# Kernel tuning notes

Hardware: AMD Instinct MI355X
Metric: run time of the kernel (lower is better)

## Reference

```python
import jax, jax.numpy as jnp
import numpy as np
from jax import lax

DIM = 96
HEADS = 3
EPS = 1e-12


def conv1x1(x, w):
    # x: [b,c,h,w], w: [o,c]
    return jnp.einsum('bchw,oc->bohw', x, w)


def dwconv3(x, w):
    # depthwise 3x3, SAME padding. w: [C,1,3,3]
    C = x.shape[1]
    return lax.conv_general_dilated(
        x, w, window_strides=(1, 1), padding='SAME',
        feature_group_count=C,
        dimension_numbers=('NCHW', 'OIHW', 'NCHW'))


def channel_attn(q, kv, temperature):
    # q: [b,C,h,w], kv: [b,2C,h,w], temperature: [heads,1,1]
    k, v = jnp.split(kv, 2, axis=1)
    b, C, h, w = q.shape
    c = C // HEADS
    r = lambda x: x.reshape(b, HEADS, c, h * w)
    q, k, v = r(q), r(k), r(v)
    # L2-normalize along the (h*w) axis (torch F.normalize semantics)
    qn = q / jnp.maximum(jnp.linalg.norm(q, axis=-1, keepdims=True), EPS)
    kn = k / jnp.maximum(jnp.linalg.norm(k, axis=-1, keepdims=True), EPS)
    attn = jnp.einsum('bhcn,bhdn->bhcd', qn, kn) * temperature  # [b,heads,c,c]
    attn = jax.nn.softmax(attn, axis=-1)
    out = jnp.einsum('bhcd,bhdn->bhcn', attn, v)
    return out.reshape(b, C, h, w)


def setup_inputs() -> dict:
    key = jax.random.key(0)
    ks = jax.random.split(key, 16)
    d = DIM
    s = lambda fan: 1.0 / np.sqrt(fan)
    inp = {
        'low': jax.random.normal(ks[0], (2, d, 256, 256), jnp.float32),
        'high': jax.random.normal(ks[1], (2, d, 256, 256), jnp.float32),
        'temperature': jnp.ones((HEADS, 1, 1), jnp.float32),
        'qc_w': jax.random.normal(ks[2], (d, d), jnp.float32) * s(d),
        'qdw_c_w': jax.random.normal(ks[3], (d, 1, 3, 3), jnp.float32) * s(9),
        'kvc_w': jax.random.normal(ks[4], (2 * d, d), jnp.float32) * s(d),
        'kvdw_c_w': jax.random.normal(ks[5], (2 * d, 1, 3, 3), jnp.float32) * s(9),
        'qt_w': jax.random.normal(ks[6], (d, d), jnp.float32) * s(d),
        'qdw_t_w': jax.random.normal(ks[7], (d, 1, 3, 3), jnp.float32) * s(9),
        'kvt_w': jax.random.normal(ks[8], (2 * d, d), jnp.float32) * s(d),
        'kvdw_t_w': jax.random.normal(ks[9], (2 * d, 1, 3, 3), jnp.float32) * s(9),
        'po_c_w': jax.random.normal(ks[10], (d, d), jnp.float32) * s(d),
        'po_t_w': jax.random.normal(ks[11], (d, d), jnp.float32) * s(d),
        'concat_w': jax.random.normal(ks[12], (d, 2 * d), jnp.float32) * s(2 * d),
        'concat_b': jax.random.normal(ks[13], (d,), jnp.float32) * s(2 * d),
    }
    return inp


def reference(low, high, temperature, qc_w, qdw_c_w, kvc_w, kvdw_c_w,
              qt_w, qdw_t_w, kvt_w, kvdw_t_w, po_c_w, po_t_w,
              concat_w, concat_b):
    q_c = dwconv3(conv1x1(high, qc_w), qdw_c_w)
    kv_c = dwconv3(conv1x1(high, kvc_w), kvdw_c_w)
    q_t = dwconv3(conv1x1(low, qt_w), qdw_t_w)
    kv_t = dwconv3(conv1x1(low, kvt_w), kvdw_t_w)
    out_c = conv1x1(channel_attn(q_c, kv_t, temperature), po_c_w)
    out_t = conv1x1(channel_attn(q_t, kv_c, temperature), po_t_w)
    out = jnp.concatenate([out_c, out_t], axis=1)
    out = conv1x1(out, concat_w) + concat_b[None, :, None, None]
    return out
```

## Files before the change

### kernel.cpp

```cpp
#include <hip/hip_runtime.h>
#include <hip/hip_bf16.h>

#define HW 65536
#define GNS 64

typedef __attribute__((ext_vector_type(8))) short short8;
typedef __attribute__((ext_vector_type(4))) float f32x4;
union U8 { short8 s; unsigned u[4]; ushort h[8]; };

static __device__ __forceinline__ ushort f2bf(float f) {
    union { float f; unsigned u; } v; v.f = f;
    unsigned u = v.u;
    unsigned r = (u + 0x7fffu + ((u >> 16) & 1u)) >> 16;
    return (ushort)r;
}
static __device__ __forceinline__ float bf2f(ushort u) {
    union { unsigned u; float f; } v; v.u = ((unsigned)u) << 16; return v.f;
}
static __device__ __forceinline__ unsigned pk2(float a, float b) {
    __hip_bfloat162 h = __float22bfloat162_rn(make_float2(a, b));
    union { __hip_bfloat162 h; unsigned u; } c; c.h = h; return c.u;
}
static __device__ __forceinline__ f32x4 mfma16(short8 a, short8 b, f32x4 c) {
    return __builtin_amdgcn_mfma_f32_16x16x32_bf16(a, b, c, 0, 0, 0);
}

__global__ __launch_bounds__(256) void prep_kernel(
        const float* __restrict__ qc, const float* __restrict__ kvc,
        const float* __restrict__ qt, const float* __restrict__ kvt,
        const float* __restrict__ cw, const float* __restrict__ poc, const float* __restrict__ pot,
        ushort* __restrict__ Wc, ushort* __restrict__ Wt,
        float* __restrict__ W1, float* __restrict__ W2, float* __restrict__ SSQ) {
    int bx = blockIdx.x, tid = threadIdx.x;
    if (bx < 9) {
        for (int idx = bx * 256 + tid; idx < 288 * 96; idx += 9 * 256) {
            Wc[idx] = f2bf(idx < 96 * 96 ? qc[idx] : kvc[idx - 96 * 96]);
            Wt[idx] = f2bf(idx < 96 * 96 ? qt[idx] : kvt[idx - 96 * 96]);
        }
        if (bx == 0)
            for (int idx = tid; idx < 8 * 96; idx += 256) SSQ[idx] = 0.f;
    } else {
        int idx = (bx - 9) * 256 + tid;
        int sel = idx < 9216 ? 0 : 1;
        int i = sel ? idx - 9216 : idx;
        int o = i / 96, m = i % 96;
        const float* po = sel ? pot : poc;
        float acc = 0.f;
        for (int p = 0; p < 96; ++p)
            acc += cw[o * 192 + sel * 96 + p] * po[p * 96 + m];
        (sel ? W2 : W1)[i] = acc;
    }
}

__global__ __launch_bounds__(256, 2) void conv_kernel(
        const float* __restrict__ Xc, const float* __restrict__ Xt,
        const ushort* __restrict__ Wcp, const ushort* __restrict__ Wtp,
        ushort* __restrict__ Yco, ushort* __restrict__ Yto) {
    __shared__ ushort xs[96][136];
    int strm = blockIdx.z;
    const float* X = strm ? Xt : Xc;
    const ushort* W = strm ? Wtp : Wcp;
    ushort* Y = strm ? Yto : Yco;
    int tid = threadIdx.x;
    int n0 = blockIdx.x * 128;
    int b = blockIdx.y;
    int wave = tid >> 6, lane = tid & 63, lr = lane & 15, lg = lane >> 4;
    const float* Xb = X + (size_t)b * 96 * HW + n0;
    #pragma unroll
    for (int i = 0; i < 12; ++i) {
        int idx = tid + i * 256;
        int ch = idx >> 5, g = idx & 31;
        float4 v = *(const float4*)(Xb + (size_t)ch * HW + 4 * g);
        unsigned* d = (unsigned*)&xs[ch][4 * g];
        d[0] = pk2(v.x, v.y);
        d[1] = pk2(v.z, v.w);
    }
    __syncthreads();
    short8 af[2][3];
    #pragma unroll
    for (int nt = 0; nt < 2; ++nt) {
        int n = wave * 32 + nt * 16 + lr;
        #pragma unroll
        for (int kk = 0; kk < 3; ++kk) {
            int kb = kk * 32 + lg * 8;
            U8 t;
            #pragma unroll
            for (int j = 0; j < 4; ++j) {
                unsigned e0 = xs[kb + 2 * j][n];
                unsigned e1 = xs[kb + 2 * j + 1][n];
                t.u[j] = e0 | (e1 << 16);
            }
            af[nt][kk] = t.s;
        }
    }
    __syncthreads();
    ushort* ys = &xs[0][0];
    int row0 = tid >> 4, g = tid & 15;
    for (int og = 0; og < 3; ++og) {
        const ushort* Wg = W + (size_t)og * 96 * 96 + (size_t)lr * 96 + lg * 8;
        #pragma unroll
        for (int mt = 0; mt < 6; ++mt) {
            f32x4 a0 = {0.f, 0.f, 0.f, 0.f}, a1 = {0.f, 0.f, 0.f, 0.f};
            #pragma unroll
            for (int kk = 0; kk < 3; ++kk) {
                short8 wf = *(const short8*)(Wg + (size_t)mt * 16 * 96 + kk * 32);
                a0 = mfma16(af[0][kk], wf, a0);
                a1 = mfma16(af[1][kk], wf, a1);
            }
            unsigned* d0 = (unsigned*)&ys[(mt * 16 + lr) * 136 + wave * 32 + lg * 4];
            d0[0] = pk2(a0[0], a0[1]);
            d0[1] = pk2(a0[2], a0[3]);
            unsigned* d1 = (unsigned*)&ys[(mt * 16 + lr) * 136 + wave * 32 + 16 + lg * 4];
            d1[0] = pk2(a1[0], a1[1]);
            d1[1] = pk2(a1[2], a1[3]);
        }
        __syncthreads();
        ushort* Yg = Y + (size_t)(b * 288 + og * 96) * HW + n0;
        #pragma unroll
        for (int p = 0; p < 6; ++p) {
            int row = p * 16 + row0;
            *(short8*)&Yg[(size_t)row * HW + 8 * g] = *(const short8*)&ys[row * 136 + 8 * g];
        }
        __syncthreads();
    }
}

__global__ __launch_bounds__(256, 8) void dw_kernel(
        const ushort* __restrict__ Yc, const ushort* __restrict__ Yt,
        const float* __restrict__ qdw_c, const float* __restrict__ kvdw_c,
        const float* __restrict__ qdw_t, const float* __restrict__ kvdw_t,
        ushort* __restrict__ QKVc, ushort* __restrict__ QKVt,
        float* __restrict__ SSQ, int base_strm) {
    int tid = threadIdx.x, wave = tid >> 6, lane = tid & 63;
    int strm = base_strm + blockIdx.z;
    int ch = blockIdx.y % 288, b = blockIdx.y / 288;
    int r0 = blockIdx.x * 32 + wave * 8;
    const ushort* Y = strm ? Yt : Yc;
    ushort* QKV = strm ? QKVt : QKVc;
    const float* qdw = strm ? qdw_t : qdw_c;
    const float* kvdw = strm ? kvdw_t : kvdw_c;
    const float* w = (ch < 96) ? (qdw + ch * 9) : (kvdw + (ch - 96) * 9);
    float w00 = w[0], w01 = w[1], w02 = w[2], w10 = w[3], w11 = w[4],
          w12 = w[5], w20 = w[6], w21 = w[7], w22 = w[8];
    const ushort* src = Y + (size_t)(b * 288 + ch) * HW;
    float rows[3][6];
    float ssq = 0.f;
    #define LOADROW(R, D)                                                    \
    {                                                                        \
        int r_ = (R);                                                        \
        if ((unsigned)r_ < 256u) {                                           \
            ushort4 t4 = *(const ushort4*)(src + r_ * 256 + 4 * lane);       \
            float c0 = bf2f(t4.x), c1 = bf2f(t4.y), c2 = bf2f(t4.z), c3 = bf2f(t4.w); \
            float lft = __shfl(c3, lane - 1);                                \
            float rgt = __shfl(c0, lane + 1);                                \
            if (lane == 0) lft = 0.f;                                        \
            if (lane == 63) rgt = 0.f;                                       \
            D[0] = lft; D[1] = c0; D[2] = c1; D[3] = c2; D[4] = c3; D[5] = rgt; \
        } else {                                                             \
            D[0] = 0.f; D[1] = 0.f; D[2] = 0.f; D[3] = 0.f; D[4] = 0.f; D[5] = 0.f; \
        }                                                                    \
    }
    LOADROW(r0 - 1, rows[0]);
    LOADROW(r0, rows[1]);
    ushort* dst = QKV + (size_t)(b * 288 + ch) * HW;
    #pragma unroll
    for (int orow = 0; orow < 8; ++orow) {
        LOADROW(r0 + orow + 1, rows[(orow + 2) % 3]);
        float* ra = rows[orow % 3];
        float* rb = rows[(orow + 1) % 3];
        float* rc = rows[(orow + 2) % 3];
        float acc[4];
        #pragma unroll
        for (int j = 0; j < 4; ++j) {
            acc[j] = w00 * ra[j] + w01 * ra[j + 1] + w02 * ra[j + 2]
                   + w10 * rb[j] + w11 * rb[j + 1] + w12 * rb[j + 2]
                   + w20 * rc[j] + w21 * rc[j + 1] + w22 * rc[j + 2];
            ssq += acc[j] * acc[j];
        }
        uint2 pv;
        pv.x = pk2(acc[0], acc[1]);
        pv.y = pk2(acc[2], acc[3]);
        *(uint2*)&dst[(r0 + orow) * 256 + 4 * lane] = pv;
    }
    #undef LOADROW
    if (ch < 192) {
        #pragma unroll
        for (int off = 1; off < 64; off <<= 1) ssq += __shfl_xor(ssq, off);
        if (lane == 0) {
            int t_ = ch >= 96;
            int chq = t_ ? ch - 96 : ch;
            int a_ = (strm == 0) ? t_ : (1 - t_);
            atomicAdd(&SSQ[((a_ * 2 + b) * 2 + t_) * 96 + chq], ssq);
        }
    }
}

__global__ __launch_bounds__(256) void gram_kernel(const ushort* __restrict__ QKVc,
                                                   const ushort* __restrict__ QKVt,
                                                   float* __restrict__ Gpart) {
    __shared__ ushort qs[32 * 256];
    __shared__ ushort ks2[32 * 256];
    __shared__ float Gp[4][32][32];
    int tid = threadIdx.x, wave = tid >> 6, lane = tid & 63;
    int lr = lane & 15, lg = lane >> 4;
    int code = blockIdx.y;
    int a = code / 6, b = (code % 6) / 3, h = code % 3;
    const ushort* qsrc = (a == 0) ? QKVc : QKVt;
    const ushort* ksrc = (a == 0) ? QKVt : QKVc;
    const ushort* qb = qsrc + (size_t)(b * 288 + 32 * h) * HW + blockIdx.x * 1024;
    const ushort* kb = ksrc + (size_t)(b * 288 + 96 + 32 * h) * HW + blockIdx.x * 1024;
    f32x4 acc[2][2];
    #pragma unroll
    for (int i = 0; i < 2; ++i)
        #pragma unroll
        for (int j = 0; j < 2; ++j) acc[i][j] = (f32x4){0.f, 0.f, 0.f, 0.f};
    for (int ph = 0; ph < 4; ++ph) {
        int noff = ph * 256;
        #pragma unroll
        for (int i = 0; i < 4; ++i) {
            int idx = tid + i * 256;
            int row = idx >> 5, g = idx & 31;
            int col = (g * 8) ^ ((row & 7) << 3);
            *(short8*)&qs[row * 256 + col] = *(const short8*)(qb + (size_t)row * HW + noff + 8 * g);
            *(short8*)&ks2[row * 256 + col] = *(const short8*)(kb + (size_t)row * HW + noff + 8 * g);
        }
        __syncthreads();
        #pragma unroll
        for (int j = 0; j < 2; ++j) {
            int ks_ = wave * 2 + j;
            int c0 = (ks_ * 32 + lg * 8) ^ ((lr & 7) << 3);
            short8 a0 = *(const short8*)&qs[lr * 256 + c0];
            short8 a1 = *(const short8*)&qs[(16 + lr) * 256 + c0];
            short8 b0 = *(const short8*)&ks2[lr * 256 + c0];
            short8 b1 = *(const short8*)&ks2[(16 + lr) * 256 + c0];
            acc[0][0] = mfma16(a0, b0, acc[0][0]);
            acc[0][1] = mfma16(a0, b1, acc[0][1]);
            acc[1][0] = mfma16(a1, b0, acc[1][0]);
            acc[1][1] = mfma16(a1, b1, acc[1][1]);
        }
        __syncthreads();
    }
    #pragma unroll
    for (int i = 0; i < 2; ++i)
        #pragma unroll
        for (int j = 0; j < 2; ++j)
            #pragma unroll
            for (int r = 0; r < 4; ++r)
                Gp[wave][i * 16 + lg * 4 + r][j * 16 + lr] = acc[i][j][r];
    __syncthreads();
    float* Gout = Gpart + ((size_t)code * GNS + blockIdx.x) * 1024;
    for (int idx = tid; idx < 1024; idx += 256) {
        float ssum = 0.f;
        #pragma unroll
        for (int wv = 0; wv < 4; ++wv) ssum += (&Gp[wv][0][0])[idx];
        Gout[idx] = ssum;
    }
}

__global__ __launch_bounds__(256) void attn_kernel(const float* __restrict__ Gpart,
                                                   const float* __restrict__ SSQ,
                                                   const float* __restrict__ temperature,
                                                   const float* __restrict__ W1,
                                                   const float* __restrict__ W2,
                                                   ushort* __restrict__ Mcat) {
    __shared__ float Gs[1024];
    __shared__ float nq[32], nk[32], A[32][32];
    int tid = threadIdx.x;
    int code = blockIdx.x;
    int a = code / 6, b = (code % 6) / 3, h = code % 3;
    const float* gp = Gpart + (size_t)code * GNS * 1024;
    #pragma unroll
    for (int j = 0; j < 4; ++j) {
        int idx = tid + j * 256;
        float s = 0.f;
        #pragma unroll 8
        for (int p = 0; p < GNS; ++p) s += gp[(size_t)p * 1024 + idx];
        Gs[idx] = s;
    }
    if (tid < 32)
        nq[tid] = fmaxf(sqrtf(fmaxf(SSQ[((a * 2 + b) * 2 + 0) * 96 + 32 * h + tid], 0.f)), 1e-12f);
    else if (tid < 64)
        nk[tid - 32] = fmaxf(sqrtf(fmaxf(SSQ[((a * 2 + b) * 2 + 1) * 96 + 32 * h + (tid - 32)], 0.f)), 1e-12f);
    __syncthreads();
    if (tid < 32) {
        float t = temperature[h];
        float lgv[32];
        float inq = t / nq[tid];
        float mx = -1e30f;
        #pragma unroll
        for (int j = 0; j < 32; ++j) { lgv[j] = Gs[tid * 32 + j] * inq / nk[j]; mx = fmaxf(mx, lgv[j]); }
        float ssum = 0.f;
        #pragma unroll
        for (int j = 0; j < 32; ++j) { lgv[j] = expf(lgv[j] - mx); ssum += lgv[j]; }
        float inv = 1.f / ssum;
        #pragma unroll
        for (int j = 0; j < 32; ++j) A[tid][j] = lgv[j] * inv;
    }
    __syncthreads();
    const float* Wm = (a == 0) ? W1 : W2;
    for (int idx = tid; idx < 96 * 32; idx += 256) {
        int o = idx >> 5, d = idx & 31;
        float acc = 0.f;
        #pragma unroll
        for (int i = 0; i < 32; ++i)
            acc += Wm[o * 96 + 32 * h + i] * A[i][d];
        Mcat[(size_t)(b * 96 + o) * 192 + a * 96 + 32 * h + d] = f2bf(acc);
    }
}

__global__ __launch_bounds__(256, 2) void final_kernel(const ushort* __restrict__ QKVc,
                                                       const ushort* __restrict__ QKVt,
                                                       const ushort* __restrict__ Mcat,
                                                       const float* __restrict__ bias,
                                                       float* __restrict__ out) {
    __shared__ float smem[96 * 132];
    ushort* vs = (ushort*)smem;
    int tid = threadIdx.x;
    int n0 = blockIdx.x * 128, b = blockIdx.y;
    int wave = tid >> 6, lane = tid & 63, lr = lane & 15, lg = lane >> 4;
    #pragma unroll
    for (int i = 0; i < 12; ++i) {
        int idx = tid + i * 256;
        int d = idx >> 4, g = idx & 15;
        const ushort* sp = (d < 96) ? (QKVt + (size_t)(b * 288 + 192 + d) * HW)
                                    : (QKVc + (size_t)(b * 288 + 192 + (d - 96)) * HW);
        U8 t;
        t.s = *(const short8*)(sp + n0 + 8 * g);
        unsigned* dst = (unsigned*)&vs[d * 132 + 8 * g];
        dst[0] = t.u[0]; dst[1] = t.u[1]; dst[2] = t.u[2]; dst[3] = t.u[3];
    }
    __syncthreads();
    short8 vf[2][6];
    #pragma unroll
    for (int nt = 0; nt < 2; ++nt) {
        int n = wave * 32 + nt * 16 + lr;
        #pragma unroll
        for (int kk = 0; kk < 6; ++kk) {
            int kb = kk * 32 + lg * 8;
            U8 t;
            #pragma unroll
            for (int j = 0; j < 4; ++j) {
                unsigned e0 = vs[(kb + 2 * j) * 132 + n];
                unsigned e1 = vs[(kb + 2 * j + 1) * 132 + n];
                t.u[j] = e0 | (e1 << 16);
            }
            vf[nt][kk] = t.s;
        }
    }
    __syncthreads();
    const ushort* Mb = Mcat + (size_t)b * 96 * 192;
    #pragma unroll
    for (int mt = 0; mt < 6; ++mt) {
        f32x4 a0 = {0.f, 0.f, 0.f, 0.f}, a1 = {0.f, 0.f, 0.f, 0.f};
        #pragma unroll
        for (int kk = 0; kk < 6; ++kk) {
            short8 mf = *(const short8*)&Mb[(size_t)(mt * 16 + lr) * 192 + kk * 32 + lg * 8];
            a0 = mfma16(vf[0][kk], mf, a0);
            a1 = mfma16(vf[1][kk], mf, a1);
        }
        *(float4*)&smem[(mt * 16 + lr) * 132 + wave * 32 + lg * 4] =
            make_float4(a0[0], a0[1], a0[2], a0[3]);
        *(float4*)&smem[(mt * 16 + lr) * 132 + wave * 32 + 16 + lg * 4] =
            make_float4(a1[0], a1[1], a1[2], a1[3]);
    }
    __syncthreads();
    float* outb = out + (size_t)b * 96 * HW + n0;
    int row0 = tid >> 5, q = tid & 31;
    #pragma unroll
    for (int p = 0; p < 12; ++p) {
        int row = p * 8 + row0;
        float4 v = *(const float4*)&smem[row * 132 + 4 * q];
        float bb = bias[row];
        v.x += bb; v.y += bb; v.z += bb; v.w += bb;
        *(float4*)&outb[(size_t)row * HW + 4 * q] = v;
    }
}

extern "C" void kernel_launch(void* const* d_in, const int* in_sizes, int n_in,
                              void* d_out, int out_size, void* d_ws, size_t ws_size,
                              hipStream_t stream) {
    const float* low    = (const float*)d_in[0];
    const float* high   = (const float*)d_in[1];
    const float* temp   = (const float*)d_in[2];
    const float* qc_w   = (const float*)d_in[3];
    const float* qdw_c  = (const float*)d_in[4];
    const float* kvc_w  = (const float*)d_in[5];
    const float* kvdw_c = (const float*)d_in[6];
    const float* qt_w   = (const float*)d_in[7];
    const float* qdw_t  = (const float*)d_in[8];
    const float* kvt_w  = (const float*)d_in[9];
    const float* kvdw_t = (const float*)d_in[10];
    const float* po_c   = (const float*)d_in[11];
    const float* po_t   = (const float*)d_in[12];
    const float* cw     = (const float*)d_in[13];
    const float* cb     = (const float*)d_in[14];
    float* out = (float*)d_out;

    char* ws = (char*)d_ws;
    const size_t SY = (size_t)2 * 288 * HW * 2;
    const size_t EXTRA = 2 * (size_t)(288 * 96 * 2) + 2 * (size_t)(96 * 96 * 4)
                       + (size_t)(8 * 96 * 4) + (size_t)(2 * 96 * 192 * 2);
    bool merged = (ws_size >= 4 * SY + EXTRA);
    size_t nbig = merged ? 4 : 3;
    ushort* B0 = (ushort*)(ws);
    ushort* B1 = (ushort*)(ws + SY);
    ushort* B2 = (ushort*)(ws + 2 * SY);
    ushort* B3 = (ushort*)(ws + 3 * SY);
    float* Gpart = (float*)ws;
    char* p = ws + nbig * SY;
    ushort* Wc = (ushort*)p; p += 288 * 96 * 2;
    ushort* Wt = (ushort*)p; p += 288 * 96 * 2;
    float* W1  = (float*)p;  p += 96 * 96 * 4;
    float* W2  = (float*)p;  p += 96 * 96 * 4;
    float* SSQ = (float*)p;  p += 8 * 96 * 4;
    ushort* Mcat = (ushort*)p; p += 2 * 96 * 192 * 2;
    if ((size_t)(p - ws) > ws_size) return;

    prep_kernel<<<81, 256, 0, stream>>>(qc_w, kvc_w, qt_w, kvt_w, cw, po_c, po_t, Wc, Wt, W1, W2, SSQ);
    ushort* QKVc;
    ushort* QKVt;
    if (merged) {
        QKVc = B2; QKVt = B3;
        conv_kernel<<<dim3(512, 2, 2), 256, 0, stream>>>(high, low, Wc, Wt, B0, B1);
        dw_kernel<<<dim3(8, 576, 2), 256, 0, stream>>>(B0, B1, qdw_c, kvdw_c, qdw_t, kvdw_t,
                                                       QKVc, QKVt, SSQ, 0);
    } else {
        QKVc = B1; QKVt = B2;
        conv_kernel<<<dim3(512, 2, 1), 256, 0, stream>>>(high, high, Wc, Wc, B0, B0);
        dw_kernel<<<dim3(8, 576, 1), 256, 0, stream>>>(B0, B0, qdw_c, kvdw_c, qdw_c, kvdw_c,
                                                       QKVc, QKVc, SSQ, 0);
        conv_kernel<<<dim3(512, 2, 1), 256, 0, stream>>>(low, low, Wt, Wt, B0, B0);
        dw_kernel<<<dim3(8, 576, 1), 256, 0, stream>>>(B0, B0, qdw_t, kvdw_t, qdw_t, kvdw_t,
                                                       QKVt, QKVt, SSQ, 1);
    }
    gram_kernel<<<dim3(GNS, 12), 256, 0, stream>>>(QKVc, QKVt, Gpart);
    attn_kernel<<<12, 256, 0, stream>>>(Gpart, SSQ, temp, W1, W2, Mcat);
    final_kernel<<<dim3(512, 2), 256, 0, stream>>>(QKVc, QKVt, Mcat, cb, out);
}
```

Before: 235.0 us.

## Overlap V depthwise conv with gram kernel and halve final kernel shared memory

In the merged path, the depthwise conv is split in two. A Q/K-only kernel runs first, and the V-channel depthwise work is folded into the gram kernel as extra blocks, so V production can overlap with the Gram reduction instead of serialising. The final kernel now stages V in two halves of 96 channels and accumulates MFMA results in registers. This halves its shared memory and should raise occupancy, at the cost of more syncs and more register pressure. The non-merged path keeps a full dw kernel and launches gram with no extra blocks.

```diff
diff --git a/kernel.cpp b/kernel.cpp
--- a/kernel.cpp
+++ b/kernel.cpp
@@ -125,15 +125,31 @@
     }
 }
 
-__global__ __launch_bounds__(256, 8) void dw_kernel(
+#define DW_LOADROW(R, D)                                                     \
+{                                                                            \
+    int r_ = (R);                                                            \
+    if ((unsigned)r_ < 256u) {                                               \
+        ushort4 t4 = *(const ushort4*)(src + r_ * 256 + 4 * lane);           \
+        float c0 = bf2f(t4.x), c1 = bf2f(t4.y), c2 = bf2f(t4.z), c3 = bf2f(t4.w); \
+        float lft = __shfl(c3, lane - 1);                                    \
+        float rgt = __shfl(c0, lane + 1);                                    \
+        if (lane == 0) lft = 0.f;                                            \
+        if (lane == 63) rgt = 0.f;                                           \
+        D[0] = lft; D[1] = c0; D[2] = c1; D[3] = c2; D[4] = c3; D[5] = rgt;  \
+    } else {                                                                 \
+        D[0] = 0.f; D[1] = 0.f; D[2] = 0.f; D[3] = 0.f; D[4] = 0.f; D[5] = 0.f; \
+    }                                                                        \
+}
+
+__global__ __launch_bounds__(256, 8) void dwqk_kernel(
         const ushort* __restrict__ Yc, const ushort* __restrict__ Yt,
         const float* __restrict__ qdw_c, const float* __restrict__ kvdw_c,
         const float* __restrict__ qdw_t, const float* __restrict__ kvdw_t,
         ushort* __restrict__ QKVc, ushort* __restrict__ QKVt,
-        float* __restrict__ SSQ, int base_strm) {
+        float* __restrict__ SSQ) {
     int tid = threadIdx.x, wave = tid >> 6, lane = tid & 63;
-    int strm = base_strm + blockIdx.z;
-    int ch = blockIdx.y % 288, b = blockIdx.y / 288;
+    int strm = blockIdx.z;
+    int ch = blockIdx.y % 192, b = blockIdx.y / 192;
     int r0 = blockIdx.x * 32 + wave * 8;
     const ushort* Y = strm ? Yt : Yc;
     ushort* QKV = strm ? QKVt : QKVc;
@@ -145,27 +161,12 @@
     const ushort* src = Y + (size_t)(b * 288 + ch) * HW;
     float rows[3][6];
     float ssq = 0.f;
-    #define LOADROW(R, D)                                                    \
-    {                                                                        \
-        int r_ = (R);                                                        \
-        if ((unsigned)r_ < 256u) {                                           \
-            ushort4 t4 = *(const ushort4*)(src + r_ * 256 + 4 * lane);       \
-            float c0 = bf2f(t4.x), c1 = bf2f(t4.y), c2 = bf2f(t4.z), c3 = bf2f(t4.w); \
-            float lft = __shfl(c3, lane - 1);                                \
-            float rgt = __shfl(c0, lane + 1);                                \
-            if (lane == 0) lft = 0.f;                                        \
-            if (lane == 63) rgt = 0.f;                                       \
-            D[0] = lft; D[1] = c0; D[2] = c1; D[3] = c2; D[4] = c3; D[5] = rgt; \
-        } else {                                                             \
-            D[0] = 0.f; D[1] = 0.f; D[2] = 0.f; D[3] = 0.f; D[4] = 0.f; D[5] = 0.f; \
-        }                                                                    \
-    }
-    LOADROW(r0 - 1, rows[0]);
-    LOADROW(r0, rows[1]);
+    DW_LOADROW(r0 - 1, rows[0]);
+    DW_LOADROW(r0, rows[1]);
     ushort* dst = QKV + (size_t)(b * 288 + ch) * HW;
     #pragma unroll
     for (int orow = 0; orow < 8; ++orow) {
-        LOADROW(r0 + orow + 1, rows[(orow + 2) % 3]);
+        DW_LOADROW(r0 + orow + 1, rows[(orow + 2) % 3]);
         float* ra = rows[orow % 3];
         float* rb = rows[(orow + 1) % 3];
         float* rc = rows[(orow + 2) % 3];
@@ -182,7 +183,51 @@
         pv.y = pk2(acc[2], acc[3]);
         *(uint2*)&dst[(r0 + orow) * 256 + 4 * lane] = pv;
     }
-    #undef LOADROW
+    #pragma unroll
+    for (int off = 1; off < 64; off <<= 1) ssq += __shfl_xor(ssq, off);
+    if (lane == 0) {
+        int t_ = ch >= 96;
+        int chq = t_ ? ch - 96 : ch;
+        int a_ = (strm == 0) ? t_ : (1 - t_);
+        atomicAdd(&SSQ[((a_ * 2 + b) * 2 + t_) * 96 + chq], ssq);
+    }
+}
+
+__global__ __launch_bounds__(256, 8) void dwfull_kernel(
+        const ushort* __restrict__ Y, const float* __restrict__ qdw,
+        const float* __restrict__ kvdw, ushort* __restrict__ QKV,
+        float* __restrict__ SSQ, int strm) {
+    int tid = threadIdx.x, wave = tid >> 6, lane = tid & 63;
+    int ch = blockIdx.y % 288, b = blockIdx.y / 288;
+    int r0 = blockIdx.x * 32 + wave * 8;
+    const float* w = (ch < 96) ? (qdw + ch * 9) : (kvdw + (ch - 96) * 9);
+    float w00 = w[0], w01 = w[1], w02 = w[2], w10 = w[3], w11 = w[4],
+          w12 = w[5], w20 = w[6], w21 = w[7], w22 = w[8];
+    const ushort* src = Y + (size_t)(b * 288 + ch) * HW;
+    float rows[3][6];
+    float ssq = 0.f;
+    DW_LOADROW(r0 - 1, rows[0]);
+    DW_LOADROW(r0, rows[1]);
+    ushort* dst = QKV + (size_t)(b * 288 + ch) * HW;
+    #pragma unroll
+    for (int orow = 0; orow < 8; ++orow) {
+        DW_LOADROW(r0 + orow + 1, rows[(orow + 2) % 3]);
+        float* ra = rows[orow % 3];
+        float* rb = rows[(orow + 1) % 3];
+        float* rc = rows[(orow + 2) % 3];
+        float acc[4];
+        #pragma unroll
+        for (int j = 0; j < 4; ++j) {
+            acc[j] = w00 * ra[j] + w01 * ra[j + 1] + w02 * ra[j + 2]
+                   + w10 * rb[j] + w11 * rb[j + 1] + w12 * rb[j + 2]
+                   + w20 * rc[j] + w21 * rc[j + 1] + w22 * rc[j + 2];
+            ssq += acc[j] * acc[j];
+        }
+        uint2 pv;
+        pv.x = pk2(acc[0], acc[1]);
+        pv.y = pk2(acc[2], acc[3]);
+        *(uint2*)&dst[(r0 + orow) * 256 + 4 * lane] = pv;
+    }
     if (ch < 192) {
         #pragma unroll
         for (int off = 1; off < 64; off <<= 1) ssq += __shfl_xor(ssq, off);
@@ -195,13 +240,52 @@
     }
 }
 
-__global__ __launch_bounds__(256) void gram_kernel(const ushort* __restrict__ QKVc,
-                                                   const ushort* __restrict__ QKVt,
-                                                   float* __restrict__ Gpart) {
+__global__ __launch_bounds__(256) void gram_dwv_kernel(
+        ushort* __restrict__ QKVc, ushort* __restrict__ QKVt,
+        float* __restrict__ Gpart,
+        const ushort* __restrict__ Yc, const ushort* __restrict__ Yt,
+        const float* __restrict__ kvdw_c, const float* __restrict__ kvdw_t,
+        int gns) {
     __shared__ ushort qs[32 * 256];
     __shared__ ushort ks2[32 * 256];
     __shared__ float Gp[4][32][32];
     int tid = threadIdx.x, wave = tid >> 6, lane = tid & 63;
+    if ((int)blockIdx.x >= gns) {
+        int flat = ((int)blockIdx.x - gns) * 12 + (int)blockIdx.y;
+        int rg = flat & 7, cc = flat >> 3;
+        int strm = cc / 192, rem = cc % 192;
+        int b = rem / 96, cv = rem % 96;
+        int r0 = rg * 32 + wave * 8;
+        const ushort* Y = strm ? Yt : Yc;
+        ushort* QKV = strm ? QKVt : QKVc;
+        const float* kvdw = strm ? kvdw_t : kvdw_c;
+        const float* w = kvdw + (96 + cv) * 9;
+        float w00 = w[0], w01 = w[1], w02 = w[2], w10 = w[3], w11 = w[4],
+              w12 = w[5], w20 = w[6], w21 = w[7], w22 = w[8];
+        const ushort* src = Y + (size_t)(b * 288 + 192 + cv) * HW;
+        float rows[3][6];
+        DW_LOADROW(r0 - 1, rows[0]);
+        DW_LOADROW(r0, rows[1]);
+        ushort* dst = QKV + (size_t)(b * 288 + 192 + cv) * HW;
+        #pragma unroll
+        for (int orow = 0; orow < 8; ++orow) {
+            DW_LOADROW(r0 + orow + 1, rows[(orow + 2) % 3]);
+            float* ra = rows[orow % 3];
+            float* rb = rows[(orow + 1) % 3];
+            float* rc = rows[(orow + 2) % 3];
+            float acc[4];
+            #pragma unroll
+            for (int j = 0; j < 4; ++j)
+                acc[j] = w00 * ra[j] + w01 * ra[j + 1] + w02 * ra[j + 2]
+                       + w10 * rb[j] + w11 * rb[j + 1] + w12 * rb[j + 2]
+                       + w20 * rc[j] + w21 * rc[j + 1] + w22 * rc[j + 2];
+            uint2 pv;
+            pv.x = pk2(acc[0], acc[1]);
+            pv.y = pk2(acc[2], acc[3]);
+            *(uint2*)&dst[(r0 + orow) * 256 + 4 * lane] = pv;
+        }
+        return;
+    }
     int lr = lane & 15, lg = lane >> 4;
     int code = blockIdx.y;
     int a = code / 6, b = (code % 6) / 3, h = code % 3;
@@ -313,66 +397,82 @@
                                                        const ushort* __restrict__ Mcat,
                                                        const float* __restrict__ bias,
                                                        float* __restrict__ out) {
-    __shared__ float smem[96 * 132];
+    __shared__ float smem[48 * 132];
     ushort* vs = (ushort*)smem;
     int tid = threadIdx.x;
     int n0 = blockIdx.x * 128, b = blockIdx.y;
     int wave = tid >> 6, lane = tid & 63, lr = lane & 15, lg = lane >> 4;
-    #pragma unroll
-    for (int i = 0; i < 12; ++i) {
-        int idx = tid + i * 256;
-        int d = idx >> 4, g = idx & 15;
-        const ushort* sp = (d < 96) ? (QKVt + (size_t)(b * 288 + 192 + d) * HW)
-                                    : (QKVc + (size_t)(b * 288 + 192 + (d - 96)) * HW);
-        U8 t;
-        t.s = *(const short8*)(sp + n0 + 8 * g);
-        unsigned* dst = (unsigned*)&vs[d * 132 + 8 * g];
-        dst[0] = t.u[0]; dst[1] = t.u[1]; dst[2] = t.u[2]; dst[3] = t.u[3];
-    }
-    __syncthreads();
-    short8 vf[2][6];
-    #pragma unroll
-    for (int nt = 0; nt < 2; ++nt) {
-        int n = wave * 32 + nt * 16 + lr;
-        #pragma unroll
-        for (int kk = 0; kk < 6; ++kk) {
-            int kb = kk * 32 + lg * 8;
+    f32x4 acc[6][2];
+    #pragma unroll
+    for (int mt = 0; mt < 6; ++mt) {
+        acc[mt][0] = (f32x4){0.f, 0.f, 0.f, 0.f};
+        acc[mt][1] = (f32x4){0.f, 0.f, 0.f, 0.f};
+    }
+    const ushort* Mb = Mcat + (size_t)b * 96 * 192;
+    for (int half = 0; half < 2; ++half) {
+        #pragma unroll
+        for (int i = 0; i < 6; ++i) {
+            int idx = tid + i * 256;
+            int dl = idx >> 4, g = idx & 15;
+            int d = half * 96 + dl;
+            const ushort* sp = (d < 96) ? (QKVt + (size_t)(b * 288 + 192 + d) * HW)
+                                        : (QKVc + (size_t)(b * 288 + 192 + (d - 96)) * HW);
             U8 t;
+            t.s = *(const short8*)(sp + n0 + 8 * g);
+            unsigned* dst = (unsigned*)&vs[dl * 132 + 8 * g];
+            dst[0] = t.u[0]; dst[1] = t.u[1]; dst[2] = t.u[2]; dst[3] = t.u[3];
+        }
+        __syncthreads();
+        short8 vf[2][3];
+        #pragma unroll
+        for (int nt = 0; nt < 2; ++nt) {
+            int n = wave * 32 + nt * 16 + lr;
             #pragma unroll
-            for (int j = 0; j < 4; ++j) {
-                unsigned e0 = vs[(kb + 2 * j) * 132 + n];
-                unsigned e1 = vs[(kb + 2 * j + 1) * 132 + n];
-                t.u[j] = e0 | (e1 << 16);
+            for (int kk = 0; kk < 3; ++kk) {
+                int kb = kk * 32 + lg * 8;
+                U8 t;
+                #pragma unroll
+                for (int j = 0; j < 4; ++j) {
+                    unsigned e0 = vs[(kb + 2 * j) * 132 + n];
+                    unsigned e1 = vs[(kb + 2 * j + 1) * 132 + n];
+                    t.u[j] = e0 | (e1 << 16);
+                }
+                vf[nt][kk] = t.s;
             }
-            vf[nt][kk] = t.s;
-        }
-    }
-    __syncthreads();
-    const ushort* Mb = Mcat + (size_t)b * 96 * 192;
-    #pragma unroll
-    for (int mt = 0; mt < 6; ++mt) {
-        f32x4 a0 = {0.f, 0.f, 0.f, 0.f}, a1 = {0.f, 0.f, 0.f, 0.f};
-        #pragma unroll
-        for (int kk = 0; kk < 6; ++kk) {
-            short8 mf = *(const short8*)&Mb[(size_t)(mt * 16 + lr) * 192 + kk * 32 + lg * 8];
-            a0 = mfma16(vf[0][kk], mf, a0);
-            a1 = mfma16(vf[1][kk], mf, a1);
-        }
-        *(float4*)&smem[(mt * 16 + lr) * 132 + wave * 32 + lg * 4] =
-            make_float4(a0[0], a0[1], a0[2], a0[3]);
-        *(float4*)&smem[(mt * 16 + lr) * 132 + wave * 32 + 16 + lg * 4] =
-            make_float4(a1[0], a1[1], a1[2], a1[3]);
-    }
-    __syncthreads();
+        }
+        __syncthreads();
+        #pragma unroll
+        for (int mt = 0; mt < 6; ++mt)
+            #pragma unroll
+            for (int kk = 0; kk < 3; ++kk) {
+                short8 mf = *(const short8*)&Mb[(size_t)(mt * 16 + lr) * 192 + half * 96 + kk * 32 + lg * 8];
+                acc[mt][0] = mfma16(vf[0][kk], mf, acc[mt][0]);
+                acc[mt][1] = mfma16(vf[1][kk], mf, acc[mt][1]);
+            }
+    }
     float* outb = out + (size_t)b * 96 * HW + n0;
-    int row0 = tid >> 5, q = tid & 31;
-    #pragma unroll
-    for (int p = 0; p < 12; ++p) {
-        int row = p * 8 + row0;
-        float4 v = *(const float4*)&smem[row * 132 + 4 * q];
-        float bb = bias[row];
-        v.x += bb; v.y += bb; v.z += bb; v.w += bb;
-        *(float4*)&outb[(size_t)row * HW + 4 * q] = v;
+    #pragma unroll
+    for (int half = 0; half < 2; ++half) {
+        #pragma unroll
+        for (int m = 0; m < 3; ++m) {
+            int mt = half * 3 + m;
+            *(float4*)&smem[(m * 16 + lr) * 132 + wave * 32 + lg * 4] =
+                make_float4(acc[mt][0][0], acc[mt][0][1], acc[mt][0][2], acc[mt][0][3]);
+            *(float4*)&smem[(m * 16 + lr) * 132 + wave * 32 + 16 + lg * 4] =
+                make_float4(acc[mt][1][0], acc[mt][1][1], acc[mt][1][2], acc[mt][1][3]);
+        }
+        __syncthreads();
+        #pragma unroll
+        for (int i = 0; i < 6; ++i) {
+            int idx = tid + i * 256;
+            int row = idx >> 5, q = idx & 31;
+            float4 v = *(const float4*)&smem[row * 132 + 4 * q];
+            int grow = half * 48 + row;
+            float bb = bias[grow];
+            v.x += bb; v.y += bb; v.z += bb; v.w += bb;
+            *(float4*)&outb[(size_t)grow * HW + 4 * q] = v;
+        }
+        __syncthreads();
     }
 }
 
@@ -422,18 +522,19 @@
     if (merged) {
         QKVc = B2; QKVt = B3;
         conv_kernel<<<dim3(512, 2, 2), 256, 0, stream>>>(high, low, Wc, Wt, B0, B1);
-        dw_kernel<<<dim3(8, 576, 2), 256, 0, stream>>>(B0, B1, qdw_c, kvdw_c, qdw_t, kvdw_t,
-                                                       QKVc, QKVt, SSQ, 0);
+        dwqk_kernel<<<dim3(8, 384, 2), 256, 0, stream>>>(B0, B1, qdw_c, kvdw_c, qdw_t, kvdw_t,
+                                                         QKVc, QKVt, SSQ);
+        gram_dwv_kernel<<<dim3(GNS + 256, 12), 256, 0, stream>>>(QKVc, QKVt, Gpart, B0, B1,
+                                                                 kvdw_c, kvdw_t, GNS);
     } else {
         QKVc = B1; QKVt = B2;
         conv_kernel<<<dim3(512, 2, 1), 256, 0, stream>>>(high, high, Wc, Wc, B0, B0);
-        dw_kernel<<<dim3(8, 576, 1), 256, 0, stream>>>(B0, B0, qdw_c, kvdw_c, qdw_c, kvdw_c,
-                                                       QKVc, QKVc, SSQ, 0);
+        dwfull_kernel<<<dim3(8, 576), 256, 0, stream>>>(B0, qdw_c, kvdw_c, QKVc, SSQ, 0);
         conv_kernel<<<dim3(512, 2, 1), 256, 0, stream>>>(low, low, Wt, Wt, B0, B0);
-        dw_kernel<<<dim3(8, 576, 1), 256, 0, stream>>>(B0, B0, qdw_t, kvdw_t, qdw_t, kvdw_t,
-                                                       QKVt, QKVt, SSQ, 1);
-    }
-    gram_kernel<<<dim3(GNS, 12), 256, 0, stream>>>(QKVc, QKVt, Gpart);
+        dwfull_kernel<<<dim3(8, 576), 256, 0, stream>>>(B0, qdw_t, kvdw_t, QKVt, SSQ, 1);
+        gram_dwv_kernel<<<dim3(GNS, 12), 256, 0, stream>>>(QKVc, QKVt, Gpart, B0, B0,
+                                                           kvdw_c, kvdw_t, GNS);
+    }
     attn_kernel<<<12, 256, 0, stream>>>(Gpart, SSQ, temp, W1, W2, Mcat);
     final_kernel<<<dim3(512, 2), 256, 0, stream>>>(QKVc, QKVt, Mcat, cb, out);
 }
```

Measured after the change: 230.5 us. About the same (-1.9%).
